# Kernel optimization log

Hardware: AMD Instinct MI355X
Metric: run time of the kernel (lower is better)

## Reference

```python
import jax, jax.numpy as jnp
import numpy as np

N, E, D = 50000, 512000, 128

def mish(x):
    return x * jnp.tanh(jax.nn.softplus(x))

def ln(x, g, b):
    m = jnp.mean(x, axis=-1, keepdims=True)
    v = jnp.var(x, axis=-1, keepdims=True)
    return (x - m) / jnp.sqrt(v + 1e-5) * g + b

def setup_inputs():
    key = jax.random.key(0)
    ks = jax.random.split(key, 16)
    W = lambda k, i, o: jax.random.normal(k, (i, o), jnp.float32) * 0.02
    z = jnp.zeros((D,), jnp.float32)
    o = jnp.ones((D,), jnp.float32)
    return {
        "node_feat": jax.random.normal(ks[0], (N, D), jnp.float32),
        "coord_feat": jax.random.normal(ks[1], (N, D), jnp.float32),
        "Wq": W(ks[2], D, D), "bq": z, "gq": o, "beq": z,
        "Wk": W(ks[3], D, D), "bk": z, "gk": o, "bek": z,
        "Wm1": W(ks[4], D, D), "bm1": z, "gm": o, "bem": z,
        "Wm2": W(ks[5], D, D), "bm2": z,
        "Wb1": W(ks[6], D, D), "bb1": z, "gb": o, "beb": z,
        "Wb2": W(ks[7], D, D), "bb2": z,
        "Ww1": W(ks[8], D, D), "bw1": z, "gw": o, "bew": z,
        "Ww2": W(ks[9], D, D), "bw2": z,
        "Wn1": W(ks[10], 2 * D, D), "bn1": z,
        "Wn2": W(ks[11], D, D), "bn2": z,
        "Wc1": W(ks[12], D, D), "bc1": z,
        "Wc2": W(ks[13], D, D),
        "src": jax.random.randint(ks[14], (E,), 0, N, jnp.int32),
        "dst": jax.random.randint(ks[15], (E,), 0, N, jnp.int32),
    }

def reference(node_feat, coord_feat, Wq, bq, gq, beq, Wk, bk, gk, bek,
              Wm1, bm1, gm, bem, Wm2, bm2, Wb1, bb1, gb, beb, Wb2, bb2,
              Ww1, bw1, gw, bew, Ww2, bw2, Wn1, bn1, Wn2, bn2, Wc1, bc1, Wc2,
              src, dst):
    # linear_q / linear_k on coord features: Linear -> LayerNorm -> Mish
    q = mish(ln(coord_feat @ Wq + bq, gq, beq))   # [N, D]
    k = mish(ln(coord_feat @ Wk + bk, gk, bek))   # [N, D]
    # u_sub_v('q','k'): per-edge q[src] - k[dst]
    rel = q[src] - k[dst]                          # [E, D]
    radial = jnp.sum(rel * rel, axis=-1, keepdims=True)  # [E, 1]
    rel = rel / jnp.sqrt(radial + 1e-8)
    # relative position encodings from dst coord features
    xd = coord_feat[dst]                           # [E, D]
    pem = mish(ln(xd @ Wm1 + bm1, gm, bem)) @ Wm2 + bm2
    peb = mish(ln(xd @ Wb1 + bb1, gb, beb)) @ Wb2 + bb2
    rel = rel * pem + peb
    # weight_encoding MLP
    w = mish(ln(rel @ Ww1 + bw1, gw, bew)) @ Ww2 + bw2  # [E, D]
    # dgl.softmax_edges over a single graph: softmax across the edge axis
    w = jax.nn.softmax(w, axis=0)
    # update_all(copy_e, sum): scatter-add edge weights to destination nodes
    h_neigh = jax.ops.segment_sum(w, dst, num_segments=N)  # [N, D]
    h = mish(jnp.concatenate([node_feat, h_neigh], axis=-1) @ Wn1 + bn1) @ Wn2 + bn2
    x = mish(coord_feat @ Wc1 + bc1) @ Wc2
    return (h, x)
```

## Files before the change

### kernel.cpp

```cpp
#include <hip/hip_runtime.h>
#include <cstdint>
#include <cstddef>

#define DN 128
#define NND 50000
#define NED 512000
#define NSCAN 49

typedef __attribute__((ext_vector_type(8))) short bf8;
typedef __attribute__((ext_vector_type(4))) float f4;
typedef unsigned short us;

__device__ __forceinline__ us f2bf(float f){
  union { float f; unsigned int u; } c; c.f = f;
  unsigned int r = c.u + 0x7fffu + ((c.u >> 16) & 1u);
  return (us)(r >> 16);
}
__device__ __forceinline__ float bf2f(us u){
  union { unsigned int u; float f; } c; c.u = ((unsigned int)u) << 16;
  return c.f;
}
__device__ __forceinline__ float mishf(float x){
  float e = __expf(x);
  float u = 1.f + e;
  float u2 = u * u;
  float t = (u2 - 1.f) / (u2 + 1.f);
  return x * ((x > 20.f) ? 1.f : t);
}

#define MFMA16(a, b, c) __builtin_amdgcn_mfma_f32_16x16x32_bf16((a), (b), (c), 0, 0, 0)

__device__ __forceinline__ bf8 lds_frag(const us* base, int row, int rowStrideB, int kElem){
  int byte = row * rowStrideB + kElem * 2;
  byte ^= (row & 7) << 4;
  return *(const bf8*)((const char*)base + byte);
}
__device__ __forceinline__ bf8 gfrag(const us* W, int n, int K, int kElem){
  return *(const bf8*)(W + (size_t)n * K + kElem);
}

template<int OUT_BF16>
__device__ __forceinline__ void store_tile(void* outp, int nrows, int r0,
                                           int wr, int wc, int g, int s, int ostride,
                                           const f4 (&A)[2][4]){
#pragma unroll
  for (int rt = 0; rt < 2; ++rt)
#pragma unroll
    for (int ct = 0; ct < 4; ++ct)
#pragma unroll
      for (int reg = 0; reg < 4; ++reg){
        int row = r0 + wr*32 + rt*16 + g*4 + reg;
        if (row < nrows){
          int col = wc*64 + ct*16 + s;
          float v = A[rt][ct][reg];
          if constexpr (OUT_BF16 != 0)
            ((us*)outp)[(size_t)row*ostride + col] = f2bf(v);
          else
            ((float*)outp)[(size_t)row*ostride + col] = v;
        }
      }
}

__device__ __forceinline__ void gemm_reg(const bf8 (&a)[2][4], const us* __restrict__ WT,
                                         const float* __restrict__ bias,
                                         int wc, int g, int s, f4 (&acc)[2][4]){
#pragma unroll
  for (int ct = 0; ct < 4; ++ct){
    float bv = bias ? bias[wc*64 + ct*16 + s] : 0.f;
    f4 t = {bv, bv, bv, bv};
    acc[0][ct] = t; acc[1][ct] = t;
  }
#pragma unroll
  for (int ct = 0; ct < 4; ++ct){
    int n = wc*64 + ct*16 + s;
#pragma unroll
    for (int kk = 0; kk < 4; ++kk){
      bf8 b = gfrag(WT, n, DN, kk*32 + g*8);
      acc[0][ct] = MFMA16(a[0][kk], b, acc[0][ct]);
      acc[1][ct] = MFMA16(a[1][kk], b, acc[1][ct]);
    }
  }
}

__device__ __forceinline__ void ln_mish(f4 (&acc)[2][4],
                                        const float* __restrict__ gam,
                                        const float* __restrict__ bet,
                                        int wr, int wc, int g, int s,
                                        float (*rowsum)[64][2], float (*rowsq)[64][2],
                                        int buf){
  float gv[4], bev[4];
#pragma unroll
  for (int ct = 0; ct < 4; ++ct){ int n = wc*64 + ct*16 + s; gv[ct] = gam[n]; bev[ct] = bet[n]; }
#pragma unroll
  for (int rt = 0; rt < 2; ++rt)
#pragma unroll
    for (int reg = 0; reg < 4; ++reg){
      float sm = acc[rt][0][reg] + acc[rt][1][reg] + acc[rt][2][reg] + acc[rt][3][reg];
      float sq = acc[rt][0][reg]*acc[rt][0][reg] + acc[rt][1][reg]*acc[rt][1][reg]
               + acc[rt][2][reg]*acc[rt][2][reg] + acc[rt][3][reg]*acc[rt][3][reg];
#pragma unroll
      for (int m = 1; m < 16; m <<= 1){ sm += __shfl_xor(sm, m, 64); sq += __shfl_xor(sq, m, 64); }
      if (s == 0){
        int row = wr*32 + rt*16 + g*4 + reg;
        rowsum[buf][row][wc] = sm; rowsq[buf][row][wc] = sq;
      }
    }
  __syncthreads();
#pragma unroll
  for (int rt = 0; rt < 2; ++rt)
#pragma unroll
    for (int reg = 0; reg < 4; ++reg){
      int row = wr*32 + rt*16 + g*4 + reg;
      float sm = rowsum[buf][row][0] + rowsum[buf][row][1];
      float sq = rowsq[buf][row][0] + rowsq[buf][row][1];
      float mu = sm * (1.f/128.f);
      float var = sq * (1.f/128.f) - mu*mu;
      float rs = rsqrtf(var + 1e-5f);
#pragma unroll
      for (int ct = 0; ct < 4; ++ct)
        acc[rt][ct][reg] = mishf((acc[rt][ct][reg] - mu) * rs * gv[ct] + bev[ct]);
    }
}

__device__ __forceinline__ void write_T(us* Tsh, int wr, int wc, int g, int s,
                                        const f4 (&A)[2][4]){
#pragma unroll
  for (int rt = 0; rt < 2; ++rt)
#pragma unroll
    for (int ct = 0; ct < 4; ++ct)
#pragma unroll
      for (int reg = 0; reg < 4; ++reg){
        int row = wr*32 + rt*16 + g*4 + reg;
        int col = wc*64 + ct*16 + s;
        int byte = row*256 + col*2; byte ^= (row & 7) << 4;
        *(us*)((char*)Tsh + byte) = f2bf(A[rt][ct][reg]);
      }
}

__device__ __forceinline__ void load_a2(const us* Tsh, int wr, int g, int s, bf8 (&a2)[2][4]){
#pragma unroll
  for (int rt = 0; rt < 2; ++rt)
#pragma unroll
    for (int kk = 0; kk < 4; ++kk)
      a2[rt][kk] = lds_frag(Tsh, wr*32 + rt*16 + s, 256, kk*32 + g*8);
}

__global__ __launch_bounds__(256, 2)
void node_fused(const float* __restrict__ X,
                const us* __restrict__ WqT,  const float* __restrict__ bq,
                const float* __restrict__ gq, const float* __restrict__ beq,
                const us* __restrict__ WkT,  const float* __restrict__ bk,
                const float* __restrict__ gk, const float* __restrict__ bek,
                const us* __restrict__ Wm1T, const float* __restrict__ bm1,
                const float* __restrict__ gm, const float* __restrict__ bem,
                const us* __restrict__ Wm2T, const float* __restrict__ bm2,
                const us* __restrict__ Wb1T, const float* __restrict__ bb1,
                const float* __restrict__ gb, const float* __restrict__ beb,
                const us* __restrict__ Wb2T, const float* __restrict__ bb2,
                const us* __restrict__ Wc1T, const float* __restrict__ bc1,
                const us* __restrict__ Wc2T,
                us* __restrict__ qt, us* __restrict__ kmb, float* __restrict__ xout)
{
  __shared__ us Ash[64 * DN];
  __shared__ float rowsum[2][64][2];
  __shared__ float rowsq[2][64][2];

  const int tid = threadIdx.x;
  const int r0 = blockIdx.x * 64;

  {
    int r = tid >> 2, c4 = tid & 3;
    int grow = r0 + r; if (grow >= NND) grow = NND - 1;
    const f4* sp = (const f4*)(X + (size_t)grow * DN + c4 * 32);
#pragma unroll
    for (int j = 0; j < 4; ++j){
      f4 v0 = sp[2*j], v1 = sp[2*j+1];
      bf8 o;
#pragma unroll
      for (int q = 0; q < 4; ++q){ o[q] = (short)f2bf(v0[q]); o[4+q] = (short)f2bf(v1[q]); }
      int byte = r*256 + c4*64 + j*16; byte ^= (r & 7) << 4;
      *(bf8*)((char*)Ash + byte) = o;
    }
  }
  __syncthreads();

  const int lane = tid & 63, w = tid >> 6;
  const int wr = w >> 1, wc = w & 1;
  const int g = lane >> 4, s = lane & 15;

  bf8 a[2][4];
#pragma unroll
  for (int rt = 0; rt < 2; ++rt)
#pragma unroll
    for (int kk = 0; kk < 4; ++kk)
      a[rt][kk] = lds_frag(Ash, wr*32 + rt*16 + s, 256, kk*32 + g*8);
  __syncthreads();

  f4 acc[2][4], acc2[2][4];
  bf8 a2[2][4];

  gemm_reg(a, WqT, bq, wc, g, s, acc);
  ln_mish(acc, gq, beq, wr, wc, g, s, rowsum, rowsq, 0);
  store_tile<1>((void*)qt, NND, r0, wr, wc, g, s, DN, acc);

  gemm_reg(a, WkT, bk, wc, g, s, acc);
  ln_mish(acc, gk, bek, wr, wc, g, s, rowsum, rowsq, 1);
  store_tile<1>((void*)kmb, NND, r0, wr, wc, g, s, 384, acc);

  gemm_reg(a, Wm1T, bm1, wc, g, s, acc);
  ln_mish(acc, gm, bem, wr, wc, g, s, rowsum, rowsq, 0);
  write_T(Ash, wr, wc, g, s, acc);
  __syncthreads();
  load_a2(Ash, wr, g, s, a2);
#pragma unroll
  for (int ct = 0; ct < 4; ++ct){
    float bv = bm2[wc*64 + ct*16 + s]; f4 t = {bv,bv,bv,bv}; acc2[0][ct] = t; acc2[1][ct] = t;
  }
#pragma unroll
  for (int ct = 0; ct < 4; ++ct){
    int n = wc*64 + ct*16 + s;
#pragma unroll
    for (int kk = 0; kk < 4; ++kk){
      bf8 b = gfrag(Wm2T, n, DN, kk*32 + g*8);
      acc2[0][ct] = MFMA16(a2[0][kk], b, acc2[0][ct]);
      acc2[1][ct] = MFMA16(a2[1][kk], b, acc2[1][ct]);
    }
  }
  store_tile<1>((void*)(kmb + 128), NND, r0, wr, wc, g, s, 384, acc2);

  gemm_reg(a, Wb1T, bb1, wc, g, s, acc);
  ln_mish(acc, gb, beb, wr, wc, g, s, rowsum, rowsq, 1);
  write_T(Ash, wr, wc, g, s, acc);
  __syncthreads();
  load_a2(Ash, wr, g, s, a2);
#pragma unroll
  for (int ct = 0; ct < 4; ++ct){
    float bv = bb2[wc*64 + ct*16 + s]; f4 t = {bv,bv,bv,bv}; acc2[0][ct] = t; acc2[1][ct] = t;
  }
#pragma unroll
  for (int ct = 0; ct < 4; ++ct){
    int n = wc*64 + ct*16 + s;
#pragma unroll
    for (int kk = 0; kk < 4; ++kk){
      bf8 b = gfrag(Wb2T, n, DN, kk*32 + g*8);
      acc2[0][ct] = MFMA16(a2[0][kk], b, acc2[0][ct]);
      acc2[1][ct] = MFMA16(a2[1][kk], b, acc2[1][ct]);
    }
  }
  store_tile<1>((void*)(kmb + 256), NND, r0, wr, wc, g, s, 384, acc2);

  gemm_reg(a, Wc1T, bc1, wc, g, s, acc);
#pragma unroll
  for (int rt = 0; rt < 2; ++rt)
#pragma unroll
    for (int ct = 0; ct < 4; ++ct)
#pragma unroll
      for (int reg = 0; reg < 4; ++reg)
        acc[rt][ct][reg] = mishf(acc[rt][ct][reg]);
  __syncthreads();
  write_T(Ash, wr, wc, g, s, acc);
  __syncthreads();
  load_a2(Ash, wr, g, s, a2);
#pragma unroll
  for (int ct = 0; ct < 4; ++ct){ f4 t = {0,0,0,0}; acc2[0][ct] = t; acc2[1][ct] = t; }
#pragma unroll
  for (int ct = 0; ct < 4; ++ct){
    int n = wc*64 + ct*16 + s;
#pragma unroll
    for (int kk = 0; kk < 4; ++kk){
      bf8 b = gfrag(Wc2T, n, DN, kk*32 + g*8);
      acc2[0][ct] = MFMA16(a2[0][kk], b, acc2[0][ct]);
      acc2[1][ct] = MFMA16(a2[1][kk], b, acc2[1][ct]);
    }
  }
  store_tile<0>((void*)xout, NND, r0, wr, wc, g, s, DN, acc2);
}

__global__ void csr_count(const int* __restrict__ dst, int* __restrict__ deg){
  int e = blockIdx.x * 256 + threadIdx.x;
  if (e < NED) atomicAdd(&deg[dst[e]], 1);
}

__global__ __launch_bounds__(1024) void csr_blocksum(const int* __restrict__ deg,
                                                     int* __restrict__ bsum){
  __shared__ int sb[1024];
  int t = threadIdx.x, idx = blockIdx.x * 1024 + t;
  sb[t] = (idx < NND) ? deg[idx] : 0;
  __syncthreads();
  for (int off = 512; off > 0; off >>= 1){
    if (t < off) sb[t] += sb[t + off];
    __syncthreads();
  }
  if (t == 0) bsum[blockIdx.x] = sb[0];
}

__global__ void csr_scanroot(const int* __restrict__ bsum, int* __restrict__ boff){
  if (threadIdx.x == 0){
    int run = 0;
    for (int b = 0; b < NSCAN; ++b){ boff[b] = run; run += bsum[b]; }
  }
}

__global__ __launch_bounds__(1024) void csr_scatter(const int* __restrict__ deg,
                                                    const int* __restrict__ boff,
                                                    int* __restrict__ fillctr){
  __shared__ int ss[1024];
  int t = threadIdx.x, idx = blockIdx.x * 1024 + t;
  int v = (idx < NND) ? deg[idx] : 0;
  ss[t] = v;
  __syncthreads();
  for (int off = 1; off < 1024; off <<= 1){
    int x = (t >= off) ? ss[t - off] : 0;
    __syncthreads();
    ss[t] += x;
    __syncthreads();
  }
  if (idx < NND){
    int p = boff[blockIdx.x] + ss[t] - v;
    fillctr[idx] = p;
  }
}

__global__ void csr_fill(const int* __restrict__ src, const int* __restrict__ dst,
                         int* __restrict__ fillctr,
                         int* __restrict__ ssorted, int* __restrict__ dsorted){
  int e = blockIdx.x * 256 + threadIdx.x;
  if (e < NED){
    int d = dst[e];
    int p = atomicAdd(&fillctr[d], 1);
    ssorted[p] = src[e];
    dsorted[p] = d;
  }
}

__global__ __launch_bounds__(256, 2)
void edge_kernel(const us* __restrict__ qtab,
                 const us* __restrict__ kmb,
                 const us* __restrict__ W1T,
                 const us* __restrict__ W2T,
                 const float* __restrict__ bw1,
                 const float* __restrict__ gwp,
                 const float* __restrict__ bewp,
                 const float* __restrict__ bw2,
                 const int* __restrict__ ssorted,
                 const int* __restrict__ dsorted,
                 float* __restrict__ hacc,
                 float* __restrict__ colsum8)
{
  __shared__ us Ash[64 * DN];
  __shared__ float rowsum[1][64][2];
  __shared__ float rowsq[1][64][2];
  __shared__ int dsh[64];

  const int tid = threadIdx.x;
  const int nchunk = gridDim.x >> 3;
  const int swz = (blockIdx.x & 7) * nchunk + (blockIdx.x >> 3);
  const int e0 = swz * 64;
  const int lane = tid & 63, w = tid >> 6;
  const int wr = w >> 1, wc = w & 1;
  const int g = lane >> 4, s = lane & 15;

  if (tid < 64) dsh[tid] = dsorted[e0 + tid];

  bf8 B1[4][4], B2[4][4];
  float b1v[4], gv[4], bev[4], b2v[4];
#pragma unroll
  for (int ct = 0; ct < 4; ++ct){
    int n = wc*64 + ct*16 + s;
#pragma unroll
    for (int kk = 0; kk < 4; ++kk){
      B1[ct][kk] = gfrag(W1T, n, DN, kk*32 + g*8);
      B2[ct][kk] = gfrag(W2T, n, DN, kk*32 + g*8);
    }
    b1v[ct] = bw1[n]; gv[ct] = gwp[n]; bev[ct] = bewp[n]; b2v[ct] = bw2[n];
  }

  {
    int r = tid >> 2, c4 = tid & 3;
    int e = e0 + r;
    int sn = ssorted[e], dn = dsorted[e];
    const bf8* qp = (const bf8*)(qtab + (size_t)sn * DN + c4 * 32);
    const us* kb = kmb + (size_t)dn * 384 + c4 * 32;
    float rel[32]; float ss = 0.f;
#pragma unroll
    for (int j = 0; j < 4; ++j){
      bf8 qv = qp[j];
      bf8 kv = *(const bf8*)(kb + j*8);
#pragma unroll
      for (int q = 0; q < 8; ++q){
        float d = bf2f((us)qv[q]) - bf2f((us)kv[q]);
        rel[j*8+q] = d; ss += d * d;
      }
    }
    ss += __shfl_xor(ss, 1, 64);
    ss += __shfl_xor(ss, 2, 64);
    float rinv = rsqrtf(ss + 1e-8f);
#pragma unroll
    for (int j = 0; j < 4; ++j){
      bf8 mv = *(const bf8*)(kb + 128 + j*8);
      bf8 bv = *(const bf8*)(kb + 256 + j*8);
      bf8 o;
#pragma unroll
      for (int q = 0; q < 8; ++q){
        float v = rel[j*8+q] * rinv * bf2f((us)mv[q]) + bf2f((us)bv[q]);
        o[q] = (short)f2bf(v);
      }
      int byte = r*256 + c4*64 + j*16; byte ^= (r & 7) << 4;
      *(bf8*)((char*)Ash + byte) = o;
    }
  }
  __syncthreads();

  f4 acc[2][4];
#pragma unroll
  for (int ct = 0; ct < 4; ++ct){ f4 t = {b1v[ct], b1v[ct], b1v[ct], b1v[ct]}; acc[0][ct] = t; acc[1][ct] = t; }
  bf8 a[2][4];
#pragma unroll
  for (int rt = 0; rt < 2; ++rt)
#pragma unroll
    for (int kk = 0; kk < 4; ++kk)
      a[rt][kk] = lds_frag(Ash, wr*32 + rt*16 + s, 256, kk*32 + g*8);
#pragma unroll
  for (int ct = 0; ct < 4; ++ct)
#pragma unroll
    for (int kk = 0; kk < 4; ++kk){
      acc[0][ct] = MFMA16(a[0][kk], B1[ct][kk], acc[0][ct]);
      acc[1][ct] = MFMA16(a[1][kk], B1[ct][kk], acc[1][ct]);
    }

#pragma unroll
  for (int rt = 0; rt < 2; ++rt)
#pragma unroll
    for (int reg = 0; reg < 4; ++reg){
      float sm = acc[rt][0][reg] + acc[rt][1][reg] + acc[rt][2][reg] + acc[rt][3][reg];
      float sq = acc[rt][0][reg]*acc[rt][0][reg] + acc[rt][1][reg]*acc[rt][1][reg]
               + acc[rt][2][reg]*acc[rt][2][reg] + acc[rt][3][reg]*acc[rt][3][reg];
#pragma unroll
      for (int m = 1; m < 16; m <<= 1){ sm += __shfl_xor(sm, m, 64); sq += __shfl_xor(sq, m, 64); }
      if (s == 0){
        int row = wr*32 + rt*16 + g*4 + reg;
        rowsum[0][row][wc] = sm; rowsq[0][row][wc] = sq;
      }
    }
  __syncthreads();
#pragma unroll
  for (int rt = 0; rt < 2; ++rt)
#pragma unroll
    for (int reg = 0; reg < 4; ++reg){
      int row = wr*32 + rt*16 + g*4 + reg;
      float sm = rowsum[0][row][0] + rowsum[0][row][1];
      float sq = rowsq[0][row][0] + rowsq[0][row][1];
      float mu = sm * (1.f/128.f);
      float var = sq * (1.f/128.f) - mu*mu;
      float rs = rsqrtf(var + 1e-5f);
#pragma unroll
      for (int ct = 0; ct < 4; ++ct)
        acc[rt][ct][reg] = mishf((acc[rt][ct][reg] - mu) * rs * gv[ct] + bev[ct]);
    }

  write_T(Ash, wr, wc, g, s, acc);
  __syncthreads();

  f4 p[2][4];
#pragma unroll
  for (int ct = 0; ct < 4; ++ct){ f4 t = {b2v[ct], b2v[ct], b2v[ct], b2v[ct]}; p[0][ct] = t; p[1][ct] = t; }
  bf8 a2[2][4];
  load_a2(Ash, wr, g, s, a2);
#pragma unroll
  for (int ct = 0; ct < 4; ++ct)
#pragma unroll
    for (int kk = 0; kk < 4; ++kk){
      p[0][ct] = MFMA16(a2[0][kk], B2[ct][kk], p[0][ct]);
      p[1][ct] = MFMA16(a2[1][kk], B2[ct][kk], p[1][ct]);
    }
#pragma unroll
  for (int rt = 0; rt < 2; ++rt)
#pragma unroll
    for (int ct = 0; ct < 4; ++ct)
#pragma unroll
      for (int reg = 0; reg < 4; ++reg)
        p[rt][ct][reg] = __expf(p[rt][ct][reg]);

  __syncthreads();

  write_T(Ash, wr, wc, g, s, p);
  __syncthreads();

  {
    int col = tid & 127, half = tid >> 7;
    int rbeg = half * 32;
    float csum = 0.f;
    int prev = dsh[rbeg];
    float run = 0.f;
#pragma unroll 8
    for (int r = rbeg; r < rbeg + 32; ++r){
      int d = dsh[r];
      int byte = r*256 + col*2; byte ^= (r & 7) << 4;
      float v = bf2f(*(const us*)((const char*)Ash + byte));
      csum += v;
      if (d != prev){
        atomicAdd(&hacc[(size_t)prev * DN + col], run);
        run = v; prev = d;
      } else {
        run += v;
      }
    }
    atomicAdd(&hacc[(size_t)prev * DN + col], run);
    atomicAdd(&colsum8[(blockIdx.x & 7) * DN + col], csum);
  }
}

__global__ __launch_bounds__(256, 2)
void final_h(const float* __restrict__ nodef,
             const float* __restrict__ hacc,
             const float* __restrict__ colsum8,
             const us* __restrict__ Wn1T,
             const float* __restrict__ bn1,
             const us* __restrict__ Wn2T,
             const float* __restrict__ bn2,
             float* __restrict__ outh)
{
  __shared__ us Ash[64 * 256];
  __shared__ float rcs[DN];

  const int tid = threadIdx.x;
  const int r0 = blockIdx.x * 64;

  if (tid < DN){
    float ssum = 0.f;
#pragma unroll
    for (int x = 0; x < 8; ++x) ssum += colsum8[x * DN + tid];
    rcs[tid] = 1.f / ssum;
  }
  __syncthreads();

  {
    int r = tid >> 2, c4 = tid & 3;
    int grow = r0 + r; if (grow >= NND) grow = NND - 1;
    const f4* np = (const f4*)(nodef + (size_t)grow * DN + c4 * 32);
    const f4* hp = (const f4*)(hacc + (size_t)grow * DN + c4 * 32);
#pragma unroll
    for (int j = 0; j < 4; ++j){
      f4 v0 = np[2*j], v1 = np[2*j+1];
      bf8 o;
#pragma unroll
      for (int q = 0; q < 4; ++q){ o[q] = (short)f2bf(v0[q]); o[4+q] = (short)f2bf(v1[q]); }
      int byte = r*512 + c4*64 + j*16; byte ^= (r & 7) << 4;
      *(bf8*)((char*)Ash + byte) = o;
      f4 h0 = hp[2*j], h1 = hp[2*j+1];
      bf8 o2;
#pragma unroll
      for (int q = 0; q < 4; ++q){
        o2[q]   = (short)f2bf(h0[q] * rcs[c4*32 + j*8 + q]);
        o2[4+q] = (short)f2bf(h1[q] * rcs[c4*32 + j*8 + 4 + q]);
      }
      int byte2 = r*512 + 256 + c4*64 + j*16; byte2 ^= (r & 7) << 4;
      *(bf8*)((char*)Ash + byte2) = o2;
    }
  }
  __syncthreads();

  const int lane = tid & 63, w = tid >> 6;
  const int wr = w >> 1, wc = w & 1;
  const int g = lane >> 4, s = lane & 15;

  float b1v[4], b2v[4];
#pragma unroll
  for (int ct = 0; ct < 4; ++ct){ int n = wc*64 + ct*16 + s; b1v[ct] = bn1[n]; b2v[ct] = bn2[n]; }

  f4 acc[2][4];
#pragma unroll
  for (int ct = 0; ct < 4; ++ct){ f4 t = {b1v[ct], b1v[ct], b1v[ct], b1v[ct]}; acc[0][ct] = t; acc[1][ct] = t; }

  bf8 a[2][8];
#pragma unroll
  for (int rt = 0; rt < 2; ++rt)
#pragma unroll
    for (int kk = 0; kk < 8; ++kk)
      a[rt][kk] = lds_frag(Ash, wr*32 + rt*16 + s, 512, kk*32 + g*8);
  __syncthreads();

#pragma unroll
  for (int ct = 0; ct < 4; ++ct){
    int n = wc*64 + ct*16 + s;
#pragma unroll
    for (int kk = 0; kk < 8; ++kk){
      bf8 b = gfrag(Wn1T, n, 256, kk*32 + g*8);
      acc[0][ct] = MFMA16(a[0][kk], b, acc[0][ct]);
      acc[1][ct] = MFMA16(a[1][kk], b, acc[1][ct]);
    }
  }

#pragma unroll
  for (int rt = 0; rt < 2; ++rt)
#pragma unroll
    for (int ct = 0; ct < 4; ++ct)
#pragma unroll
      for (int reg = 0; reg < 4; ++reg)
        acc[rt][ct][reg] = mishf(acc[rt][ct][reg]);
  write_T((us*)Ash, wr, wc, g, s, acc);
  __syncthreads();

  f4 acc2[2][4];
#pragma unroll
  for (int ct = 0; ct < 4; ++ct){ f4 t = {b2v[ct], b2v[ct], b2v[ct], b2v[ct]}; acc2[0][ct] = t; acc2[1][ct] = t; }
  bf8 a2[2][4];
  load_a2((const us*)Ash, wr, g, s, a2);
#pragma unroll
  for (int ct = 0; ct < 4; ++ct){
    int n = wc*64 + ct*16 + s;
#pragma unroll
    for (int kk = 0; kk < 4; ++kk){
      bf8 b = gfrag(Wn2T, n, DN, kk*32 + g*8);
      acc2[0][ct] = MFMA16(a2[0][kk], b, acc2[0][ct]);
      acc2[1][ct] = MFMA16(a2[1][kk], b, acc2[1][ct]);
    }
  }
  store_tile<0>((void*)outh, NND, r0, wr, wc, g, s, DN, acc2);
}

struct WPrepArgs {
  const float* w[12];
  us* wt[12];
  int K[12];
};

__global__ void prep_weights(WPrepArgs a){
  int widx = blockIdx.y;
  int K = a.K[widx];
  int idx = blockIdx.x * 256 + threadIdx.x;
  if (idx >= DN * K) return;
  int kshift = (K == 256) ? 8 : 7;
  int n = idx >> kshift;
  int k = idx & (K - 1);
  a.wt[widx][idx] = f2bf(a.w[widx][(size_t)k * DN + n]);
}

extern "C" void kernel_launch(void* const* d_in, const int* in_sizes, int n_in,
                              void* d_out, int out_size, void* d_ws, size_t ws_size,
                              hipStream_t stream) {
  const float* node_feat = (const float*)d_in[0];
  const float* coordf    = (const float*)d_in[1];
  const float* Wq  = (const float*)d_in[2];
  const float* bq  = (const float*)d_in[3];
  const float* gq  = (const float*)d_in[4];
  const float* beq = (const float*)d_in[5];
  const float* Wk  = (const float*)d_in[6];
  const float* bk  = (const float*)d_in[7];
  const float* gk  = (const float*)d_in[8];
  const float* bek = (const float*)d_in[9];
  const float* Wm1 = (const float*)d_in[10];
  const float* bm1 = (const float*)d_in[11];
  const float* gm  = (const float*)d_in[12];
  const float* bem = (const float*)d_in[13];
  const float* Wm2 = (const float*)d_in[14];
  const float* bm2 = (const float*)d_in[15];
  const float* Wb1 = (const float*)d_in[16];
  const float* bb1 = (const float*)d_in[17];
  const float* gb  = (const float*)d_in[18];
  const float* beb = (const float*)d_in[19];
  const float* Wb2 = (const float*)d_in[20];
  const float* bb2 = (const float*)d_in[21];
  const float* Ww1 = (const float*)d_in[22];
  const float* bw1 = (const float*)d_in[23];
  const float* gw  = (const float*)d_in[24];
  const float* bew = (const float*)d_in[25];
  const float* Ww2 = (const float*)d_in[26];
  const float* bw2 = (const float*)d_in[27];
  const float* Wn1 = (const float*)d_in[28];
  const float* bn1 = (const float*)d_in[29];
  const float* Wn2 = (const float*)d_in[30];
  const float* bn2 = (const float*)d_in[31];
  const float* Wc1 = (const float*)d_in[32];
  const float* bc1 = (const float*)d_in[33];
  const float* Wc2 = (const float*)d_in[34];
  const int* srcI  = (const int*)d_in[35];
  const int* dstI  = (const int*)d_in[36];

  char* ws = (char*)d_ws;
  size_t off = 0;
  auto alloc = [&](size_t bytes) -> char* {
    char* p = ws + off;
    off += (bytes + 255) & ~(size_t)255;
    return p;
  };
  us*    qt      = (us*)alloc((size_t)NND * DN * 2);
  us*    kmb     = (us*)alloc((size_t)NND * 384 * 2);
  float* hacc    = (float*)alloc((size_t)NND * DN * 4);
  float* colsum8 = (float*)alloc(8 * DN * 4);
  int*   deg     = (int*)alloc((size_t)NND * 4);
  int*   fillctr = (int*)alloc((size_t)NND * 4);
  int*   ssorted = (int*)alloc((size_t)NED * 4);
  int*   dsorted = (int*)alloc((size_t)NED * 4);
  int*   bsum    = (int*)alloc((size_t)NSCAN * 4);
  int*   boff    = (int*)alloc((size_t)NSCAN * 4);
  us*    wtb     = (us*)alloc((size_t)12 * 16384 * 2);

  hipMemsetAsync(hacc, 0, (size_t)NND * DN * 4 + 8 * DN * 4, stream);
  hipMemsetAsync(deg, 0, (size_t)NND * 4, stream);

  WPrepArgs pa;
  const float* wsrc[12] = {Wq, Wk, Wm1, Wm2, Wb1, Wb2, Ww1, Ww2, Wc1, Wc2, Wn2, Wn1};
  for (int i = 0; i < 12; ++i){
    pa.w[i] = wsrc[i];
    pa.wt[i] = wtb + (size_t)i * 16384;
    pa.K[i] = (i == 11) ? 256 : 128;
  }
  prep_weights<<<dim3(128, 12), 256, 0, stream>>>(pa);

  csr_count<<<(NED + 255) / 256, 256, 0, stream>>>(dstI, deg);
  csr_blocksum<<<NSCAN, 1024, 0, stream>>>(deg, bsum);
  csr_scanroot<<<1, 64, 0, stream>>>(bsum, boff);
  csr_scatter<<<NSCAN, 1024, 0, stream>>>(deg, boff, fillctr);
  csr_fill<<<(NED + 255) / 256, 256, 0, stream>>>(srcI, dstI, fillctr, ssorted, dsorted);

  const int NB = (NND + 63) / 64;

  node_fused<<<NB, 256, 0, stream>>>(coordf,
      pa.wt[0], bq, gq, beq,
      pa.wt[1], bk, gk, bek,
      pa.wt[2], bm1, gm, bem, pa.wt[3], bm2,
      pa.wt[4], bb1, gb, beb, pa.wt[5], bb2,
      pa.wt[8], bc1, pa.wt[9],
      qt, kmb, (float*)d_out + (size_t)NND * DN);

  edge_kernel<<<NED / 64, 256, 0, stream>>>(qt, kmb, pa.wt[6], pa.wt[7],
                                            bw1, gw, bew, bw2, ssorted, dsorted,
                                            hacc, colsum8);

  final_h<<<NB, 256, 0, stream>>>(node_feat, hacc, colsum8,
                                  pa.wt[11], bn1, pa.wt[10], bn2, (float*)d_out);
}
```

Before: 517.1 us.

## Give each wave its own 16-row tile to drop block-level syncs

Each wave now owns a full 16-row by 128-column tile instead of the 2x2 wave grid sharing 64 rows. LayerNorm row reductions finish with in-wave shuffles, and each wave has a private LDS staging buffer, so __syncthreads and cross-wave rowsum exchanges go away in the node, edge and output kernels. The edge kernel also drops the LDS transpose before the segmented scatter, does the run-length atomics straight from registers, and uses a shuffle reduction for the column sums. In exchange, each weight fragment is read from global/L2 by every wave rather than shared across two. The edge kernel also no longer preloads weights into registers, and with only four rows per run there may be more atomics.

New measurement: 717.5 us. +38.8%, slower.

```diff
diff --git a/kernel.cpp b/kernel.cpp
--- a/kernel.cpp
+++ b/kernel.cpp
@@ -39,110 +39,90 @@
   return *(const bf8*)(W + (size_t)n * K + kElem);
 }
 
+
+__device__ __forceinline__ void loadA16(const us* T, int g, int s, bf8 (&a)[4]){
+#pragma unroll
+  for (int kk = 0; kk < 4; ++kk)
+    a[kk] = lds_frag(T, s, 256, kk*32 + g*8);
+}
+
+__device__ __forceinline__ void gemm8(const bf8 (&a)[4], const us* __restrict__ WT,
+                                      const float* __restrict__ bias,
+                                      int g, int s, f4 (&acc)[8]){
+#pragma unroll
+  for (int ct = 0; ct < 8; ++ct){
+    float bv = bias ? bias[ct*16 + s] : 0.f;
+    f4 t = {bv, bv, bv, bv};
+    acc[ct] = t;
+  }
+#pragma unroll
+  for (int ct = 0; ct < 8; ++ct){
+    int n = ct*16 + s;
+#pragma unroll
+    for (int kk = 0; kk < 4; ++kk)
+      acc[ct] = MFMA16(a[kk], gfrag(WT, n, DN, kk*32 + g*8), acc[ct]);
+  }
+}
+
+__device__ __forceinline__ void ln_mish8(f4 (&acc)[8],
+                                         const float* __restrict__ gam,
+                                         const float* __restrict__ bet, int s){
+  float mu[4], rs[4];
+#pragma unroll
+  for (int reg = 0; reg < 4; ++reg){
+    float sm = 0.f, sq = 0.f;
+#pragma unroll
+    for (int ct = 0; ct < 8; ++ct){ float v = acc[ct][reg]; sm += v; sq += v*v; }
+#pragma unroll
+    for (int m = 1; m < 16; m <<= 1){ sm += __shfl_xor(sm, m, 64); sq += __shfl_xor(sq, m, 64); }
+    float mm = sm * (1.f/128.f);
+    float var = sq * (1.f/128.f) - mm*mm;
+    mu[reg] = mm; rs[reg] = rsqrtf(var + 1e-5f);
+  }
+#pragma unroll
+  for (int ct = 0; ct < 8; ++ct){
+    float gv = gam[ct*16 + s], bv = bet[ct*16 + s];
+#pragma unroll
+    for (int reg = 0; reg < 4; ++reg)
+      acc[ct][reg] = mishf((acc[ct][reg] - mu[reg]) * rs[reg] * gv + bv);
+  }
+}
+
+__device__ __forceinline__ void mish8(f4 (&acc)[8]){
+#pragma unroll
+  for (int ct = 0; ct < 8; ++ct)
+#pragma unroll
+    for (int reg = 0; reg < 4; ++reg)
+      acc[ct][reg] = mishf(acc[ct][reg]);
+}
+
+__device__ __forceinline__ void writeT16(us* T, int g, int s, const f4 (&A)[8]){
+#pragma unroll
+  for (int ct = 0; ct < 8; ++ct)
+#pragma unroll
+    for (int reg = 0; reg < 4; ++reg){
+      int row = g*4 + reg, col = ct*16 + s;
+      int byte = row*256 + col*2; byte ^= (row & 7) << 4;
+      *(us*)((char*)T + byte) = f2bf(A[ct][reg]);
+    }
+}
+
 template<int OUT_BF16>
-__device__ __forceinline__ void store_tile(void* outp, int nrows, int r0,
-                                           int wr, int wc, int g, int s, int ostride,
-                                           const f4 (&A)[2][4]){
-#pragma unroll
-  for (int rt = 0; rt < 2; ++rt)
-#pragma unroll
-    for (int ct = 0; ct < 4; ++ct)
-#pragma unroll
-      for (int reg = 0; reg < 4; ++reg){
-        int row = r0 + wr*32 + rt*16 + g*4 + reg;
-        if (row < nrows){
-          int col = wc*64 + ct*16 + s;
-          float v = A[rt][ct][reg];
-          if constexpr (OUT_BF16 != 0)
-            ((us*)outp)[(size_t)row*ostride + col] = f2bf(v);
-          else
-            ((float*)outp)[(size_t)row*ostride + col] = v;
-        }
-      }
-}
-
-__device__ __forceinline__ void gemm_reg(const bf8 (&a)[2][4], const us* __restrict__ WT,
-                                         const float* __restrict__ bias,
-                                         int wc, int g, int s, f4 (&acc)[2][4]){
-#pragma unroll
-  for (int ct = 0; ct < 4; ++ct){
-    float bv = bias ? bias[wc*64 + ct*16 + s] : 0.f;
-    f4 t = {bv, bv, bv, bv};
-    acc[0][ct] = t; acc[1][ct] = t;
-  }
-#pragma unroll
-  for (int ct = 0; ct < 4; ++ct){
-    int n = wc*64 + ct*16 + s;
-#pragma unroll
-    for (int kk = 0; kk < 4; ++kk){
-      bf8 b = gfrag(WT, n, DN, kk*32 + g*8);
-      acc[0][ct] = MFMA16(a[0][kk], b, acc[0][ct]);
-      acc[1][ct] = MFMA16(a[1][kk], b, acc[1][ct]);
-    }
-  }
-}
-
-__device__ __forceinline__ void ln_mish(f4 (&acc)[2][4],
-                                        const float* __restrict__ gam,
-                                        const float* __restrict__ bet,
-                                        int wr, int wc, int g, int s,
-                                        float (*rowsum)[64][2], float (*rowsq)[64][2],
-                                        int buf){
-  float gv[4], bev[4];
-#pragma unroll
-  for (int ct = 0; ct < 4; ++ct){ int n = wc*64 + ct*16 + s; gv[ct] = gam[n]; bev[ct] = bet[n]; }
-#pragma unroll
-  for (int rt = 0; rt < 2; ++rt)
+__device__ __forceinline__ void store16(void* outp, int row0, int g, int s, int ostride,
+                                        const f4 (&A)[8]){
+#pragma unroll
+  for (int ct = 0; ct < 8; ++ct)
 #pragma unroll
     for (int reg = 0; reg < 4; ++reg){
-      float sm = acc[rt][0][reg] + acc[rt][1][reg] + acc[rt][2][reg] + acc[rt][3][reg];
-      float sq = acc[rt][0][reg]*acc[rt][0][reg] + acc[rt][1][reg]*acc[rt][1][reg]
-               + acc[rt][2][reg]*acc[rt][2][reg] + acc[rt][3][reg]*acc[rt][3][reg];
-#pragma unroll
-      for (int m = 1; m < 16; m <<= 1){ sm += __shfl_xor(sm, m, 64); sq += __shfl_xor(sq, m, 64); }
-      if (s == 0){
-        int row = wr*32 + rt*16 + g*4 + reg;
-        rowsum[buf][row][wc] = sm; rowsq[buf][row][wc] = sq;
+      int row = row0 + g*4 + reg;
+      if (row < NND){
+        int col = ct*16 + s;
+        if constexpr (OUT_BF16 != 0)
+          ((us*)outp)[(size_t)row*ostride + col] = f2bf(A[ct][reg]);
+        else
+          ((float*)outp)[(size_t)row*ostride + col] = A[ct][reg];
       }
     }
-  __syncthreads();
-#pragma unroll
-  for (int rt = 0; rt < 2; ++rt)
-#pragma unroll
-    for (int reg = 0; reg < 4; ++reg){
-      int row = wr*32 + rt*16 + g*4 + reg;
-      float sm = rowsum[buf][row][0] + rowsum[buf][row][1];
-      float sq = rowsq[buf][row][0] + rowsq[buf][row][1];
-      float mu = sm * (1.f/128.f);
-      float var = sq * (1.f/128.f) - mu*mu;
-      float rs = rsqrtf(var + 1e-5f);
-#pragma unroll
-      for (int ct = 0; ct < 4; ++ct)
-        acc[rt][ct][reg] = mishf((acc[rt][ct][reg] - mu) * rs * gv[ct] + bev[ct]);
-    }
-}
-
-__device__ __forceinline__ void write_T(us* Tsh, int wr, int wc, int g, int s,
-                                        const f4 (&A)[2][4]){
-#pragma unroll
-  for (int rt = 0; rt < 2; ++rt)
-#pragma unroll
-    for (int ct = 0; ct < 4; ++ct)
-#pragma unroll
-      for (int reg = 0; reg < 4; ++reg){
-        int row = wr*32 + rt*16 + g*4 + reg;
-        int col = wc*64 + ct*16 + s;
-        int byte = row*256 + col*2; byte ^= (row & 7) << 4;
-        *(us*)((char*)Tsh + byte) = f2bf(A[rt][ct][reg]);
-      }
-}
-
-__device__ __forceinline__ void load_a2(const us* Tsh, int wr, int g, int s, bf8 (&a2)[2][4]){
-#pragma unroll
-  for (int rt = 0; rt < 2; ++rt)
-#pragma unroll
-    for (int kk = 0; kk < 4; ++kk)
-      a2[rt][kk] = lds_frag(Tsh, wr*32 + rt*16 + s, 256, kk*32 + g*8);
 }
 
 __global__ __launch_bounds__(256, 2)
@@ -161,16 +141,17 @@
                 const us* __restrict__ Wc2T,
                 us* __restrict__ qt, us* __restrict__ kmb, float* __restrict__ xout)
 {
-  __shared__ us Ash[64 * DN];
-  __shared__ float rowsum[2][64][2];
-  __shared__ float rowsq[2][64][2];
+  __shared__ us Tsh[4][16 * DN];
 
   const int tid = threadIdx.x;
-  const int r0 = blockIdx.x * 64;
+  const int lane = tid & 63, w = tid >> 6;
+  const int g = lane >> 4, s = lane & 15;
+  const int r = lane >> 2, c4 = lane & 3;
+  const int row0 = blockIdx.x * 64 + w * 16;
+  us* T = (us*)Tsh[w];
 
   {
-    int r = tid >> 2, c4 = tid & 3;
-    int grow = r0 + r; if (grow >= NND) grow = NND - 1;
+    int grow = row0 + r; if (grow >= NND) grow = NND - 1;
     const f4* sp = (const f4*)(X + (size_t)grow * DN + c4 * 32);
 #pragma unroll
     for (int j = 0; j < 4; ++j){
@@ -179,101 +160,42 @@
 #pragma unroll
       for (int q = 0; q < 4; ++q){ o[q] = (short)f2bf(v0[q]); o[4+q] = (short)f2bf(v1[q]); }
       int byte = r*256 + c4*64 + j*16; byte ^= (r & 7) << 4;
-      *(bf8*)((char*)Ash + byte) = o;
+      *(bf8*)((char*)T + byte) = o;
     }
   }
-  __syncthreads();
-
-  const int lane = tid & 63, w = tid >> 6;
-  const int wr = w >> 1, wc = w & 1;
-  const int g = lane >> 4, s = lane & 15;
-
-  bf8 a[2][4];
-#pragma unroll
-  for (int rt = 0; rt < 2; ++rt)
-#pragma unroll
-    for (int kk = 0; kk < 4; ++kk)
-      a[rt][kk] = lds_frag(Ash, wr*32 + rt*16 + s, 256, kk*32 + g*8);
-  __syncthreads();
-
-  f4 acc[2][4], acc2[2][4];
-  bf8 a2[2][4];
-
-  gemm_reg(a, WqT, bq, wc, g, s, acc);
-  ln_mish(acc, gq, beq, wr, wc, g, s, rowsum, rowsq, 0);
-  store_tile<1>((void*)qt, NND, r0, wr, wc, g, s, DN, acc);
-
-  gemm_reg(a, WkT, bk, wc, g, s, acc);
-  ln_mish(acc, gk, bek, wr, wc, g, s, rowsum, rowsq, 1);
-  store_tile<1>((void*)kmb, NND, r0, wr, wc, g, s, 384, acc);
-
-  gemm_reg(a, Wm1T, bm1, wc, g, s, acc);
-  ln_mish(acc, gm, bem, wr, wc, g, s, rowsum, rowsq, 0);
-  write_T(Ash, wr, wc, g, s, acc);
-  __syncthreads();
-  load_a2(Ash, wr, g, s, a2);
-#pragma unroll
-  for (int ct = 0; ct < 4; ++ct){
-    float bv = bm2[wc*64 + ct*16 + s]; f4 t = {bv,bv,bv,bv}; acc2[0][ct] = t; acc2[1][ct] = t;
-  }
-#pragma unroll
-  for (int ct = 0; ct < 4; ++ct){
-    int n = wc*64 + ct*16 + s;
-#pragma unroll
-    for (int kk = 0; kk < 4; ++kk){
-      bf8 b = gfrag(Wm2T, n, DN, kk*32 + g*8);
-      acc2[0][ct] = MFMA16(a2[0][kk], b, acc2[0][ct]);
-      acc2[1][ct] = MFMA16(a2[1][kk], b, acc2[1][ct]);
-    }
-  }
-  store_tile<1>((void*)(kmb + 128), NND, r0, wr, wc, g, s, 384, acc2);
-
-  gemm_reg(a, Wb1T, bb1, wc, g, s, acc);
-  ln_mish(acc, gb, beb, wr, wc, g, s, rowsum, rowsq, 1);
-  write_T(Ash, wr, wc, g, s, acc);
-  __syncthreads();
-  load_a2(Ash, wr, g, s, a2);
-#pragma unroll
-  for (int ct = 0; ct < 4; ++ct){
-    float bv = bb2[wc*64 + ct*16 + s]; f4 t = {bv,bv,bv,bv}; acc2[0][ct] = t; acc2[1][ct] = t;
-  }
-#pragma unroll
-  for (int ct = 0; ct < 4; ++ct){
-    int n = wc*64 + ct*16 + s;
-#pragma unroll
-    for (int kk = 0; kk < 4; ++kk){
-      bf8 b = gfrag(Wb2T, n, DN, kk*32 + g*8);
-      acc2[0][ct] = MFMA16(a2[0][kk], b, acc2[0][ct]);
-      acc2[1][ct] = MFMA16(a2[1][kk], b, acc2[1][ct]);
-    }
-  }
-  store_tile<1>((void*)(kmb + 256), NND, r0, wr, wc, g, s, 384, acc2);
-
-  gemm_reg(a, Wc1T, bc1, wc, g, s, acc);
-#pragma unroll
-  for (int rt = 0; rt < 2; ++rt)
-#pragma unroll
-    for (int ct = 0; ct < 4; ++ct)
-#pragma unroll
-      for (int reg = 0; reg < 4; ++reg)
-        acc[rt][ct][reg] = mishf(acc[rt][ct][reg]);
-  __syncthreads();
-  write_T(Ash, wr, wc, g, s, acc);
-  __syncthreads();
-  load_a2(Ash, wr, g, s, a2);
-#pragma unroll
-  for (int ct = 0; ct < 4; ++ct){ f4 t = {0,0,0,0}; acc2[0][ct] = t; acc2[1][ct] = t; }
-#pragma unroll
-  for (int ct = 0; ct < 4; ++ct){
-    int n = wc*64 + ct*16 + s;
-#pragma unroll
-    for (int kk = 0; kk < 4; ++kk){
-      bf8 b = gfrag(Wc2T, n, DN, kk*32 + g*8);
-      acc2[0][ct] = MFMA16(a2[0][kk], b, acc2[0][ct]);
-      acc2[1][ct] = MFMA16(a2[1][kk], b, acc2[1][ct]);
-    }
-  }
-  store_tile<0>((void*)xout, NND, r0, wr, wc, g, s, DN, acc2);
+
+  bf8 a[4], a2[4];
+  loadA16(T, g, s, a);
+  f4 acc[8], acc2[8];
+
+  gemm8(a, WqT, bq, g, s, acc);
+  ln_mish8(acc, gq, beq, s);
+  store16<1>((void*)qt, row0, g, s, DN, acc);
+
+  gemm8(a, WkT, bk, g, s, acc);
+  ln_mish8(acc, gk, bek, s);
+  store16<1>((void*)kmb, row0, g, s, 384, acc);
+
+  gemm8(a, Wm1T, bm1, g, s, acc);
+  ln_mish8(acc, gm, bem, s);
+  writeT16(T, g, s, acc);
+  loadA16(T, g, s, a2);
+  gemm8(a2, Wm2T, bm2, g, s, acc2);
+  store16<1>((void*)(kmb + 128), row0, g, s, 384, acc2);
+
+  gemm8(a, Wb1T, bb1, g, s, acc);
+  ln_mish8(acc, gb, beb, s);
+  writeT16(T, g, s, acc);
+  loadA16(T, g, s, a2);
+  gemm8(a2, Wb2T, bb2, g, s, acc2);
+  store16<1>((void*)(kmb + 256), row0, g, s, 384, acc2);
+
+  gemm8(a, Wc1T, bc1, g, s, acc);
+  mish8(acc);
+  writeT16(T, g, s, acc);
+  loadA16(T, g, s, a2);
+  gemm8(a2, Wc2T, nullptr, g, s, acc2);
+  store16<0>((void*)xout, row0, g, s, DN, acc2);
 }
 
 __global__ void csr_count(const int* __restrict__ dst, int* __restrict__ deg){
@@ -347,166 +269,96 @@
                  float* __restrict__ hacc,
                  float* __restrict__ colsum8)
 {
-  __shared__ us Ash[64 * DN];
-  __shared__ float rowsum[1][64][2];
-  __shared__ float rowsq[1][64][2];
-  __shared__ int dsh[64];
+  __shared__ us Tsh[4][16 * DN];
 
   const int tid = threadIdx.x;
+  const int lane = tid & 63, w = tid >> 6;
+  const int g = lane >> 4, s = lane & 15;
+  const int r = lane >> 2, c4 = lane & 3;
+
   const int nchunk = gridDim.x >> 3;
   const int swz = (blockIdx.x & 7) * nchunk + (blockIdx.x >> 3);
-  const int e0 = swz * 64;
-  const int lane = tid & 63, w = tid >> 6;
-  const int wr = w >> 1, wc = w & 1;
-  const int g = lane >> 4, s = lane & 15;
-
-  if (tid < 64) dsh[tid] = dsorted[e0 + tid];
-
-  bf8 B1[4][4], B2[4][4];
-  float b1v[4], gv[4], bev[4], b2v[4];
-#pragma unroll
-  for (int ct = 0; ct < 4; ++ct){
-    int n = wc*64 + ct*16 + s;
-#pragma unroll
-    for (int kk = 0; kk < 4; ++kk){
-      B1[ct][kk] = gfrag(W1T, n, DN, kk*32 + g*8);
-      B2[ct][kk] = gfrag(W2T, n, DN, kk*32 + g*8);
+  const int e0 = swz * 64 + w * 16;
+  us* T = (us*)Tsh[w];
+
+  const int e = e0 + r;
+  const int sn = ssorted[e], dn = dsorted[e];
+  const bf8* qp = (const bf8*)(qtab + (size_t)sn * DN + c4 * 32);
+  const us*  kb = kmb + (size_t)dn * 384 + c4 * 32;
+  bf8 qv[4], kv[4], mv[4], bv[4];
+#pragma unroll
+  for (int j = 0; j < 4; ++j){
+    qv[j] = qp[j];
+    kv[j] = *(const bf8*)(kb + j*8);
+    mv[j] = *(const bf8*)(kb + 128 + j*8);
+    bv[j] = *(const bf8*)(kb + 256 + j*8);
+  }
+
+  float ss = 0.f;
+#pragma unroll
+  for (int j = 0; j < 4; ++j)
+#pragma unroll
+    for (int q = 0; q < 8; ++q){
+      float d = bf2f((us)qv[j][q]) - bf2f((us)kv[j][q]);
+      ss += d * d;
     }
-    b1v[ct] = bw1[n]; gv[ct] = gwp[n]; bev[ct] = bewp[n]; b2v[ct] = bw2[n];
-  }
-
-  {
-    int r = tid >> 2, c4 = tid & 3;
-    int e = e0 + r;
-    int sn = ssorted[e], dn = dsorted[e];
-    const bf8* qp = (const bf8*)(qtab + (size_t)sn * DN + c4 * 32);
-    const us* kb = kmb + (size_t)dn * 384 + c4 * 32;
-    float rel[32]; float ss = 0.f;
-#pragma unroll
-    for (int j = 0; j < 4; ++j){
-      bf8 qv = qp[j];
-      bf8 kv = *(const bf8*)(kb + j*8);
-#pragma unroll
-      for (int q = 0; q < 8; ++q){
-        float d = bf2f((us)qv[q]) - bf2f((us)kv[q]);
-        rel[j*8+q] = d; ss += d * d;
-      }
+  ss += __shfl_xor(ss, 1, 64);
+  ss += __shfl_xor(ss, 2, 64);
+  float rinv = rsqrtf(ss + 1e-8f);
+
+#pragma unroll
+  for (int j = 0; j < 4; ++j){
+    bf8 o;
+#pragma unroll
+    for (int q = 0; q < 8; ++q){
+      float d = bf2f((us)qv[j][q]) - bf2f((us)kv[j][q]);
+      float v = d * rinv * bf2f((us)mv[j][q]) + bf2f((us)bv[j][q]);
+      o[q] = (short)f2bf(v);
     }
-    ss += __shfl_xor(ss, 1, 64);
-    ss += __shfl_xor(ss, 2, 64);
-    float rinv = rsqrtf(ss + 1e-8f);
-#pragma unroll
-    for (int j = 0; j < 4; ++j){
-      bf8 mv = *(const bf8*)(kb + 128 + j*8);
-      bf8 bv = *(const bf8*)(kb + 256 + j*8);
-      bf8 o;
-#pragma unroll
-      for (int q = 0; q < 8; ++q){
-        float v = rel[j*8+q] * rinv * bf2f((us)mv[q]) + bf2f((us)bv[q]);
-        o[q] = (short)f2bf(v);
-      }
-      int byte = r*256 + c4*64 + j*16; byte ^= (r & 7) << 4;
-      *(bf8*)((char*)Ash + byte) = o;
-    }
-  }
-  __syncthreads();
-
-  f4 acc[2][4];
-#pragma unroll
-  for (int ct = 0; ct < 4; ++ct){ f4 t = {b1v[ct], b1v[ct], b1v[ct], b1v[ct]}; acc[0][ct] = t; acc[1][ct] = t; }
-  bf8 a[2][4];
-#pragma unroll
-  for (int rt = 0; rt < 2; ++rt)
-#pragma unroll
-    for (int kk = 0; kk < 4; ++kk)
-      a[rt][kk] = lds_frag(Ash, wr*32 + rt*16 + s, 256, kk*32 + g*8);
-#pragma unroll
-  for (int ct = 0; ct < 4; ++ct)
-#pragma unroll
-    for (int kk = 0; kk < 4; ++kk){
-      acc[0][ct] = MFMA16(a[0][kk], B1[ct][kk], acc[0][ct]);
-      acc[1][ct] = MFMA16(a[1][kk], B1[ct][kk], acc[1][ct]);
-    }
-
-#pragma unroll
-  for (int rt = 0; rt < 2; ++rt)
-#pragma unroll
-    for (int reg = 0; reg < 4; ++reg){
-      float sm = acc[rt][0][reg] + acc[rt][1][reg] + acc[rt][2][reg] + acc[rt][3][reg];
-      float sq = acc[rt][0][reg]*acc[rt][0][reg] + acc[rt][1][reg]*acc[rt][1][reg]
-               + acc[rt][2][reg]*acc[rt][2][reg] + acc[rt][3][reg]*acc[rt][3][reg];
-#pragma unroll
-      for (int m = 1; m < 16; m <<= 1){ sm += __shfl_xor(sm, m, 64); sq += __shfl_xor(sq, m, 64); }
-      if (s == 0){
-        int row = wr*32 + rt*16 + g*4 + reg;
-        rowsum[0][row][wc] = sm; rowsq[0][row][wc] = sq;
-      }
-    }
-  __syncthreads();
-#pragma unroll
-  for (int rt = 0; rt < 2; ++rt)
-#pragma unroll
-    for (int reg = 0; reg < 4; ++reg){
-      int row = wr*32 + rt*16 + g*4 + reg;
-      float sm = rowsum[0][row][0] + rowsum[0][row][1];
-      float sq = rowsq[0][row][0] + rowsq[0][row][1];
-      float mu = sm * (1.f/128.f);
-      float var = sq * (1.f/128.f) - mu*mu;
-      float rs = rsqrtf(var + 1e-5f);
-#pragma unroll
-      for (int ct = 0; ct < 4; ++ct)
-        acc[rt][ct][reg] = mishf((acc[rt][ct][reg] - mu) * rs * gv[ct] + bev[ct]);
-    }
-
-  write_T(Ash, wr, wc, g, s, acc);
-  __syncthreads();
-
-  f4 p[2][4];
-#pragma unroll
-  for (int ct = 0; ct < 4; ++ct){ f4 t = {b2v[ct], b2v[ct], b2v[ct], b2v[ct]}; p[0][ct] = t; p[1][ct] = t; }
-  bf8 a2[2][4];
-  load_a2(Ash, wr, g, s, a2);
-#pragma unroll
-  for (int ct = 0; ct < 4; ++ct)
-#pragma unroll
-    for (int kk = 0; kk < 4; ++kk){
-      p[0][ct] = MFMA16(a2[0][kk], B2[ct][kk], p[0][ct]);
-      p[1][ct] = MFMA16(a2[1][kk], B2[ct][kk], p[1][ct]);
-    }
-#pragma unroll
-  for (int rt = 0; rt < 2; ++rt)
-#pragma unroll
-    for (int ct = 0; ct < 4; ++ct)
-#pragma unroll
-      for (int reg = 0; reg < 4; ++reg)
-        p[rt][ct][reg] = __expf(p[rt][ct][reg]);
-
-  __syncthreads();
-
-  write_T(Ash, wr, wc, g, s, p);
-  __syncthreads();
-
-  {
-    int col = tid & 127, half = tid >> 7;
-    int rbeg = half * 32;
-    float csum = 0.f;
-    int prev = dsh[rbeg];
-    float run = 0.f;
-#pragma unroll 8
-    for (int r = rbeg; r < rbeg + 32; ++r){
-      int d = dsh[r];
-      int byte = r*256 + col*2; byte ^= (r & 7) << 4;
-      float v = bf2f(*(const us*)((const char*)Ash + byte));
-      csum += v;
-      if (d != prev){
-        atomicAdd(&hacc[(size_t)prev * DN + col], run);
-        run = v; prev = d;
-      } else {
-        run += v;
-      }
-    }
+    int byte = r*256 + c4*64 + j*16; byte ^= (r & 7) << 4;
+    *(bf8*)((char*)T + byte) = o;
+  }
+
+  bf8 a[4];
+  loadA16(T, g, s, a);
+  f4 acc[8];
+  gemm8(a, W1T, bw1, g, s, acc);
+
+  ln_mish8(acc, gwp, bewp, s);
+
+  writeT16(T, g, s, acc);
+  bf8 a2[4];
+  loadA16(T, g, s, a2);
+  f4 p[8];
+  gemm8(a2, W2T, bw2, g, s, p);
+#pragma unroll
+  for (int ct = 0; ct < 8; ++ct)
+#pragma unroll
+    for (int reg = 0; reg < 4; ++reg)
+      p[ct][reg] = __expf(p[ct][reg]);
+
+  const int d0 = __shfl(dn, (g*4 + 0) * 4, 64);
+  const int d1 = __shfl(dn, (g*4 + 1) * 4, 64);
+  const int d2 = __shfl(dn, (g*4 + 2) * 4, 64);
+  const int d3 = __shfl(dn, (g*4 + 3) * 4, 64);
+
+  const int cslice = (blockIdx.x & 7) * DN;
+#pragma unroll
+  for (int ct = 0; ct < 8; ++ct){
+    int col = ct*16 + s;
+    float run = p[ct][0]; int prev = d0;
+    if (d1 != prev){ atomicAdd(&hacc[(size_t)prev * DN + col], run); run = p[ct][1]; prev = d1; }
+    else run += p[ct][1];
+    if (d2 != prev){ atomicAdd(&hacc[(size_t)prev * DN + col], run); run = p[ct][2]; prev = d2; }
+    else run += p[ct][2];
+    if (d3 != prev){ atomicAdd(&hacc[(size_t)prev * DN + col], run); run = p[ct][3]; prev = d3; }
+    else run += p[ct][3];
     atomicAdd(&hacc[(size_t)prev * DN + col], run);
-    atomicAdd(&colsum8[(blockIdx.x & 7) * DN + col], csum);
+
+    float cs = p[ct][0] + p[ct][1] + p[ct][2] + p[ct][3];
+    cs += __shfl_xor(cs, 16, 64);
+    cs += __shfl_xor(cs, 32, 64);
+    if (g == 0) atomicAdd(&colsum8[cslice + col], cs);
   }
 }
 
@@ -520,11 +372,15 @@
              const float* __restrict__ bn2,
              float* __restrict__ outh)
 {
-  __shared__ us Ash[64 * 256];
+  __shared__ us Csh[4][16 * 256];
   __shared__ float rcs[DN];
 
   const int tid = threadIdx.x;
-  const int r0 = blockIdx.x * 64;
+  const int lane = tid & 63, w = tid >> 6;
+  const int g = lane >> 4, s = lane & 15;
+  const int r = lane >> 2, c4 = lane & 3;
+  const int row0 = blockIdx.x * 64 + w * 16;
+  us* C = (us*)Csh[w];
 
   if (tid < DN){
     float ssum = 0.f;
@@ -535,8 +391,7 @@
   __syncthreads();
 
   {
-    int r = tid >> 2, c4 = tid & 3;
-    int grow = r0 + r; if (grow >= NND) grow = NND - 1;
+    int grow = row0 + r; if (grow >= NND) grow = NND - 1;
     const f4* np = (const f4*)(nodef + (size_t)grow * DN + c4 * 32);
     const f4* hp = (const f4*)(hacc + (size_t)grow * DN + c4 * 32);
 #pragma unroll
@@ -546,7 +401,7 @@
 #pragma unroll
       for (int q = 0; q < 4; ++q){ o[q] = (short)f2bf(v0[q]); o[4+q] = (short)f2bf(v1[q]); }
       int byte = r*512 + c4*64 + j*16; byte ^= (r & 7) << 4;
-      *(bf8*)((char*)Ash + byte) = o;
+      *(bf8*)((char*)C + byte) = o;
       f4 h0 = hp[2*j], h1 = hp[2*j+1];
       bf8 o2;
 #pragma unroll
@@ -555,68 +410,35 @@
         o2[4+q] = (short)f2bf(h1[q] * rcs[c4*32 + j*8 + 4 + q]);
       }
       int byte2 = r*512 + 256 + c4*64 + j*16; byte2 ^= (r & 7) << 4;
-      *(bf8*)((char*)Ash + byte2) = o2;
+      *(bf8*)((char*)C + byte2) = o2;
     }
   }
-  __syncthreads();
-
-  const int lane = tid & 63, w = tid >> 6;
-  const int wr = w >> 1, wc = w & 1;
-  const int g = lane >> 4, s = lane & 15;
-
-  float b1v[4], b2v[4];
-#pragma unroll
-  for (int ct = 0; ct < 4; ++ct){ int n = wc*64 + ct*16 + s; b1v[ct] = bn1[n]; b2v[ct] = bn2[n]; }
-
-  f4 acc[2][4];
-#pragma unroll
-  for (int ct = 0; ct < 4; ++ct){ f4 t = {b1v[ct], b1v[ct], b1v[ct], b1v[ct]}; acc[0][ct] = t; acc[1][ct] = t; }
-
-  bf8 a[2][8];
-#pragma unroll
-  for (int rt = 0; rt < 2; ++rt)
+
+  bf8 a[8];
+#pragma unroll
+  for (int kk = 0; kk < 8; ++kk)
+    a[kk] = lds_frag(C, s, 512, kk*32 + g*8);
+
+  f4 acc[8];
+#pragma unroll
+  for (int ct = 0; ct < 8; ++ct){
+    float bv = bn1[ct*16 + s]; f4 t = {bv,bv,bv,bv}; acc[ct] = t;
+  }
+#pragma unroll
+  for (int ct = 0; ct < 8; ++ct){
+    int n = ct*16 + s;
 #pragma unroll
     for (int kk = 0; kk < 8; ++kk)
-      a[rt][kk] = lds_frag(Ash, wr*32 + rt*16 + s, 512, kk*32 + g*8);
-  __syncthreads();
-
-#pragma unroll
-  for (int ct = 0; ct < 4; ++ct){
-    int n = wc*64 + ct*16 + s;
-#pragma unroll
-    for (int kk = 0; kk < 8; ++kk){
-      bf8 b = gfrag(Wn1T, n, 256, kk*32 + g*8);
-      acc[0][ct] = MFMA16(a[0][kk], b, acc[0][ct]);
-      acc[1][ct] = MFMA16(a[1][kk], b, acc[1][ct]);
-    }
-  }
-
-#pragma unroll
-  for (int rt = 0; rt < 2; ++rt)
-#pragma unroll
-    for (int ct = 0; ct < 4; ++ct)
-#pragma unroll
-      for (int reg = 0; reg < 4; ++reg)
-        acc[rt][ct][reg] = mishf(acc[rt][ct][reg]);
-  write_T((us*)Ash, wr, wc, g, s, acc);
-  __syncthreads();
-
-  f4 acc2[2][4];
-#pragma unroll
-  for (int ct = 0; ct < 4; ++ct){ f4 t = {b2v[ct], b2v[ct], b2v[ct], b2v[ct]}; acc2[0][ct] = t; acc2[1][ct] = t; }
-  bf8 a2[2][4];
-  load_a2((const us*)Ash, wr, g, s, a2);
-#pragma unroll
-  for (int ct = 0; ct < 4; ++ct){
-    int n = wc*64 + ct*16 + s;
-#pragma unroll
-    for (int kk = 0; kk < 4; ++kk){
-      bf8 b = gfrag(Wn2T, n, DN, kk*32 + g*8);
-      acc2[0][ct] = MFMA16(a2[0][kk], b, acc2[0][ct]);
-      acc2[1][ct] = MFMA16(a2[1][kk], b, acc2[1][ct]);
-    }
-  }
-  store_tile<0>((void*)outh, NND, r0, wr, wc, g, s, DN, acc2);
+      acc[ct] = MFMA16(a[kk], gfrag(Wn1T, n, 256, kk*32 + g*8), acc[ct]);
+  }
+  mish8(acc);
+
+  writeT16(C, g, s, acc);
+  bf8 a2[4];
+  loadA16(C, g, s, a2);
+  f4 acc2[8];
+  gemm8(a2, Wn2T, bn2, g, s, acc2);
+  store16<0>((void*)outh, row0, g, s, DN, acc2);
 }
 
 struct WPrepArgs {
```
